# Performance work log

Hardware: AMD Instinct MI355X
Metric: run time of the kernel (lower is better)

## Reference

```python
import jax, jax.numpy as jnp
import numpy as np
import math

B, S, H = 2, 2048, 1024
NH, DK, DV = 16, 64, 64
PAD = 0
VOCAB = 32000


def setup_inputs() -> dict:
    key = jax.random.key(0)
    ks = jax.random.split(key, 6)
    batch = jax.random.normal(ks[0], (B, S, H), dtype=jnp.float32)
    input_ids = jax.random.randint(ks[1], (B, S), 1, VOCAB)
    n_pad = S // 20
    input_ids = input_ids.at[:, S - n_pad:].set(PAD)
    init = 1.0 / math.sqrt(H)  # xavier-ish scale
    W_Q = jax.random.normal(ks[2], (H, NH * DK), dtype=jnp.float32) * init
    W_K = jax.random.normal(ks[3], (H, NH * DK), dtype=jnp.float32) * init
    W_V = jax.random.normal(ks[4], (H, NH * DV), dtype=jnp.float32) * init
    W_O = jax.random.normal(ks[5], (NH * DV, H), dtype=jnp.float32) * init
    return {
        "batch": batch, "input_ids": input_ids,
        "W_Q": W_Q, "W_K": W_K, "W_V": W_V,
        "b_Q": jnp.zeros((NH * DK,), jnp.float32),
        "b_K": jnp.zeros((NH * DK,), jnp.float32),
        "b_V": jnp.zeros((NH * DV,), jnp.float32),
        "W_O": W_O, "b_O": jnp.zeros((H,), jnp.float32),
    }


def reference(batch, input_ids, W_Q, W_K, W_V, b_Q, b_K, b_V, W_O, b_O):
    Bn, Sn, _ = batch.shape
    NEG = jnp.float32(-jnp.inf)
    # causal mask [S,S]: 0 where i>=j else -inf
    i = jnp.arange(Sn)
    causal = jnp.where(i[:, None] >= i[None, :], 0.0, NEG).astype(batch.dtype)
    # padding mask [B,1,S]: -inf at pad key positions
    pad = jnp.where(input_ids == PAD, NEG, 0.0).astype(batch.dtype)
    mask = causal[None, :, :] + pad[:, None, :]  # [B,S,S]

    Q = (batch @ W_Q + b_Q).reshape(Bn, Sn, NH, DK)
    K = (batch @ W_K + b_K).reshape(Bn, Sn, NH, DK)
    V = (batch @ W_V + b_V).reshape(Bn, Sn, NH, DV)

    scores = jnp.einsum('bqhd,bkhd->bhqk', Q, K) / math.sqrt(DK)
    attn = jax.nn.softmax(scores + mask[:, None, :, :], axis=-1)
    out = jnp.einsum('bhqk,bkhd->bqhd', attn, V).reshape(Bn, Sn, NH * DV)
    return out @ W_O + b_O
```

## Files before the change

kernel.cpp:

```cpp
#include <hip/hip_runtime.h>
#include <stdint.h>


typedef unsigned short u16;
typedef __attribute__((ext_vector_type(8))) __bf16 bf16x8;
typedef __attribute__((ext_vector_type(4))) float f32x4;

#define SCL 0.18033688011112042f

__device__ __forceinline__ u16 f2bf(float f) {
  union { float f; uint32_t u; } v; v.f = f;
  uint32_t r = v.u + 0x7FFFu + ((v.u >> 16) & 1u);
  return (u16)(r >> 16);
}

__device__ __forceinline__ void gl_lds16(const u16* g, u16* l) {
  auto gp = reinterpret_cast<const __attribute__((address_space(1))) uint32_t*>(
      reinterpret_cast<uintptr_t>(g));
  auto lp = reinterpret_cast<__attribute__((address_space(3))) uint32_t*>(
      reinterpret_cast<uintptr_t>(l));
  __builtin_amdgcn_global_load_lds(gp, lp, 16, 0, 0);
}

__global__ void k_prologue(const float* __restrict__ batch, const int* __restrict__ ids,
                           const float* __restrict__ W_Q, const float* __restrict__ W_K,
                           const float* __restrict__ W_V, const float* __restrict__ W_O,
                           u16* __restrict__ Xbf, u16* __restrict__ dqkv, u16* __restrict__ dwo,
                           unsigned long long* __restrict__ pb) {
  __shared__ float tile[32][33];
  const int bx = blockIdx.x, t = threadIdx.x;
  if (bx < 4096) {
    int idx = (bx * 256 + t) * 4;
    const float4 v = *reinterpret_cast<const float4*>(batch + idx);
    uint2 o;
    o.x = (uint32_t)f2bf(v.x) | ((uint32_t)f2bf(v.y) << 16);
    o.y = (uint32_t)f2bf(v.z) | ((uint32_t)f2bf(v.w) << 16);
    *reinterpret_cast<uint2*>(Xbf + idx) = o;
  } else if (bx < 8192) {
    int b2 = bx - 4096;
    int z = b2 >> 10;
    b2 &= 1023;
    const float* src = z == 0 ? W_Q : (z == 1 ? W_K : (z == 2 ? W_V : W_O));
    u16* dst = z < 3 ? dqkv + (size_t)z * 1024 * 1024 : dwo;
    int c0 = (b2 & 31) * 32, r0 = (b2 >> 5) * 32;
    int tx = t & 31, ty = t >> 5;
#pragma unroll
    for (int i = 0; i < 4; ++i)
      tile[ty + i * 8][tx] = src[(size_t)(r0 + ty + i * 8) * 1024 + c0 + tx];
    __syncthreads();
#pragma unroll
    for (int i = 0; i < 4; ++i)
      dst[(size_t)(c0 + ty + i * 8) * 1024 + r0 + tx] = f2bf(tile[tx][ty + i * 8]);
  } else {
    int idx = (bx - 8192) * 4 + (t >> 6);
    int ln = t & 63;
    int b = idx >> 5, j = idx & 31;
    unsigned long long m = __ballot(ids[b * 2048 + j * 64 + ln] == 0);
    if (ln == 0) pb[idx] = m;
  }
}


__device__ __forceinline__ void gemm_tile_acc(
    const u16* __restrict__ A, const u16* __restrict__ Bt, int K,
    int tm, int tn, u16* As, u16* Bs, f32x4 acc[4][4]) {
  const int t = threadIdx.x, wv = t >> 6, ln = t & 63;
  const int wr = (wv & 1) * 64, wc = (wv >> 1) * 64;
  const int lr = ln & 15, q8 = (ln >> 4) * 8;
  const int srow = ln >> 2, scol = (ln & 3) * 8;

  for (int k0 = 0; k0 < K; k0 += 32) {
#pragma unroll
    for (int i = 0; i < 2; ++i) {
      int c = wv + i * 4;
      gl_lds16(A + (size_t)(tm + c * 16 + srow) * K + k0 + scol, As + c * 512 + ln * 8);
      gl_lds16(Bt + (size_t)(tn + c * 16 + srow) * K + k0 + scol, Bs + c * 512 + ln * 8);
    }
    __syncthreads();
    bf16x8 av[4], bv[4];
#pragma unroll
    for (int m = 0; m < 4; ++m)
      av[m] = *reinterpret_cast<const bf16x8*>(As + (wr + m * 16 + lr) * 32 + q8);
#pragma unroll
    for (int n = 0; n < 4; ++n)
      bv[n] = *reinterpret_cast<const bf16x8*>(Bs + (wc + n * 16 + lr) * 32 + q8);
#pragma unroll
    for (int m = 0; m < 4; ++m)
#pragma unroll
      for (int n = 0; n < 4; ++n)
        acc[m][n] = __builtin_amdgcn_mfma_f32_16x16x32_bf16(av[m], bv[n], acc[m][n], 0, 0, 0);
    __syncthreads();
  }
}

__global__ __launch_bounds__(256) void k_qkv(
    const u16* __restrict__ X, const u16* __restrict__ Wt,
    const float* __restrict__ bQ, const float* __restrict__ bK, const float* __restrict__ bV,
    u16* __restrict__ Qt, u16* __restrict__ Kt, u16* __restrict__ Vt) {
  __shared__ __align__(16) u16 As[128 * 32];
  __shared__ __align__(16) u16 Bs[128 * 32];
  f32x4 acc[4][4] = {};
  const int tm = blockIdx.x * 128, tn = blockIdx.y * 128;
  gemm_tile_acc(X, Wt, 1024, tm, tn, As, Bs, acc);

  const int t = threadIdx.x, wv = t >> 6, ln = t & 63;
  const int wr = (wv & 1) * 64, wc = (wv >> 1) * 64;
  const int lr = ln & 15, q4 = (ln >> 4) * 4;
  const int which = tn >> 10;

  if (which == 0) {
#pragma unroll
    for (int n = 0; n < 4; ++n) {
      int f = (tn + wc + n * 16 + lr) & 1023;
      float bb = bQ[f];
      int h = f >> 6, dd = f & 63;
      int kh = dd >> 5, qq = (dd & 31) >> 3, e = dd & 7;
#pragma unroll
      for (int m = 0; m < 4; ++m)
#pragma unroll
        for (int r = 0; r < 4; ++r) {
          int gr = tm + wr + m * 16 + q4 + r;
          int b = gr >> 11, s = gr & 2047;
          int bh = b * 16 + h;
          size_t addr = (((size_t)(bh * 64 + (s >> 5)) * 4 + ((s & 31) >> 4) * 2 + kh) << 9) +
                        ((s & 15) + 16 * qq) * 8 + e;
          Qt[addr] = f2bf((acc[m][n][r] + bb) * SCL);
        }
    }
  } else if (which == 1) {
#pragma unroll
    for (int n = 0; n < 4; ++n) {
      int f = (tn + wc + n * 16 + lr) & 1023;
      float bb = bK[f];
      int h = f >> 6, dd = f & 63;
      int kh = dd >> 5, qq = (dd & 31) >> 3, e = dd & 7;
#pragma unroll
      for (int m = 0; m < 4; ++m)
#pragma unroll
        for (int r = 0; r < 4; ++r) {
          int gr = tm + wr + m * 16 + q4 + r;
          int b = gr >> 11, s = gr & 2047;
          int bh = b * 16 + h;
          size_t addr = (((size_t)(bh * 32 + (s >> 6)) * 8 + kh * 4 + ((s & 63) >> 4)) << 9) +
                        ((s & 15) + 16 * qq) * 8 + e;
          Kt[addr] = f2bf(acc[m][n][r] + bb);
        }
    }
  } else {
#pragma unroll
    for (int n = 0; n < 4; ++n) {
      int f = (tn + wc + n * 16 + lr) & 1023;
      float bb = bV[f];
      int h = f >> 6, dd = f & 63;
      int md = dd >> 4, lrv = dd & 15;
#pragma unroll
      for (int m = 0; m < 4; ++m) {
        int gr0 = tm + wr + m * 16 + q4;
        int b = gr0 >> 11, s0 = gr0 & 2047;
        int bh = b * 16 + h;
        int j = s0 >> 6, kh = (s0 & 63) >> 5, qv = (s0 & 31) >> 3, e0 = s0 & 7;
        size_t addr = (((size_t)(bh * 32 + j) * 8 + kh * 4 + md) << 9) +
                      (lrv + 16 * qv) * 8 + e0;
        uint2 pk;
        pk.x = (uint32_t)f2bf(acc[m][n][0] + bb) | ((uint32_t)f2bf(acc[m][n][1] + bb) << 16);
        pk.y = (uint32_t)f2bf(acc[m][n][2] + bb) | ((uint32_t)f2bf(acc[m][n][3] + bb) << 16);
        *reinterpret_cast<uint2*>(Vt + addr) = pk;
      }
    }
  }
}

__global__ __launch_bounds__(256) void k_out(
    const u16* __restrict__ O, const u16* __restrict__ WoT,
    const float* __restrict__ bO, float* __restrict__ out) {
  __shared__ __align__(16) u16 As[128 * 32];
  __shared__ __align__(16) u16 Bs[128 * 32];
  f32x4 acc[4][4] = {};
  const int tm = blockIdx.x * 128, tn = blockIdx.y * 128;
  gemm_tile_acc(O, WoT, 1024, tm, tn, As, Bs, acc);

  const int t = threadIdx.x, wv = t >> 6, ln = t & 63;
  const int wr = (wv & 1) * 64, wc = (wv >> 1) * 64;
  const int lr = ln & 15, q4 = (ln >> 4) * 4;
#pragma unroll
  for (int n = 0; n < 4; ++n) {
    int gc = tn + wc + n * 16 + lr;
    float bb = bO[gc];
#pragma unroll
    for (int m = 0; m < 4; ++m)
#pragma unroll
      for (int r = 0; r < 4; ++r) {
        int gr = tm + wr + m * 16 + q4 + r;
        out[(size_t)gr * 1024 + gc] = acc[m][n][r] + bb;
      }
  }
}

__global__ __launch_bounds__(256, 3) void k_attn(
    const u16* __restrict__ Qt, const u16* __restrict__ Kt, const u16* __restrict__ Vt,
    const unsigned long long* __restrict__ padbits,
    u16* __restrict__ Opart, float* __restrict__ Lpart) {
  __shared__ __align__(16) u16 Ks[2][4096];
  __shared__ __align__(16) u16 Vs[2][4096];
  __shared__ __align__(16) u16 Ps[128 * 72];

  const int id = blockIdx.x;
  const int bh = id & 31;
  const int w = 39 - (id >> 5);
  int p, c;
  if (w < 4)       { p = w;                    c = 0; }
  else if (w < 12) { p = 4 + ((w - 4) >> 1);   c = (w - 4) & 1; }
  else if (w < 24) { p = 8 + (w - 12) / 3;     c = (w - 12) % 3; }
  else             { p = 12 + ((w - 24) >> 2); c = (w - 24) & 3; }
  const int jts = c * 8;
  const int jte = min(2 * p + 2, jts + 8);
  const int slot = bh * 40 + w;
  const int bI = bh >> 4;

  const int t = threadIdx.x, wv = t >> 6, ln = t & 63;
  const int lr = ln & 15, q4 = (ln >> 4) * 4, q8 = (ln >> 4) * 8;
  const int qbase = p * 128 + wv * 32;
  const int qrow = wv * 32;

  bf16x8 bq[2][2];
  {
    const u16* qb = Qt + (((size_t)(bh * 64 + (qbase >> 5)) * 4) << 9) + ln * 8;
#pragma unroll
    for (int n = 0; n < 2; ++n)
#pragma unroll
      for (int kh = 0; kh < 2; ++kh)
        bq[n][kh] = *reinterpret_cast<const bf16x8*>(qb + ((n * 2 + kh) << 9));
  }

  float lo[2] = {0.f, 0.f};
  f32x4 Oc[4][2] = {};

  const u16* Kg = Kt + (((size_t)bh * 32) << 12);
  const u16* Vg = Vt + (((size_t)bh * 32) << 12);
  const int st = t * 8;

#pragma unroll
  for (int r = 0; r < 2; ++r) {
    gl_lds16(Kg + (((size_t)jts) << 12) + st + r * 2048, &Ks[0][st + r * 2048]);
    gl_lds16(Vg + (((size_t)jts) << 12) + st + r * 2048, &Vs[0][st + r * 2048]);
  }
  __syncthreads();

  for (int j = jts; j < jte; ++j) {
    const int cur = (j - jts) & 1, nxt = cur ^ 1;
    if (j + 1 < jte) {
#pragma unroll
      for (int r = 0; r < 2; ++r) {
        gl_lds16(Kg + (((size_t)(j + 1)) << 12) + st + r * 2048, &Ks[nxt][st + r * 2048]);
        gl_lds16(Vg + (((size_t)(j + 1)) << 12) + st + r * 2048, &Vs[nxt][st + r * 2048]);
      }
    }

    const int kb = j * 64;
    const unsigned long long pb = padbits[bI * 32 + j];
    const bool masked = (kb + 63 > qbase) || (pb != 0);

    f32x4 sc[4][2] = {};
#pragma unroll
    for (int m = 0; m < 4; ++m) {
      const bf16x8 ak0 = *reinterpret_cast<const bf16x8*>(&Ks[cur][m * 512 + ln * 8]);
      const bf16x8 ak1 = *reinterpret_cast<const bf16x8*>(&Ks[cur][(4 + m) * 512 + ln * 8]);
#pragma unroll
      for (int n = 0; n < 2; ++n) {
        sc[m][n] = __builtin_amdgcn_mfma_f32_16x16x32_bf16(ak0, bq[n][0], sc[m][n], 0, 0, 0);
        sc[m][n] = __builtin_amdgcn_mfma_f32_16x16x32_bf16(ak1, bq[n][1], sc[m][n], 0, 0, 0);
      }
    }

#pragma unroll
    for (int n = 0; n < 2; ++n) {
      if (masked) {
        const int qabs = qbase + n * 16 + lr;
#pragma unroll
        for (int m = 0; m < 4; ++m)
#pragma unroll
          for (int r = 0; r < 4; ++r) {
            const int sl = m * 16 + q4 + r;
            const bool dead = (kb + sl > qabs) || ((pb >> sl) & 1ull);
            sc[m][n][r] = dead ? -1e30f : sc[m][n][r];
          }
      }
      float ps = 0.f;
#pragma unroll
      for (int m = 0; m < 4; ++m) {
        float p0 = exp2f(sc[m][n][0]);
        float p1 = exp2f(sc[m][n][1]);
        float p2 = exp2f(sc[m][n][2]);
        float p3 = exp2f(sc[m][n][3]);
        ps += (p0 + p1) + (p2 + p3);
        uint2 pk;
        pk.x = __builtin_amdgcn_perm(__float_as_uint(p1), __float_as_uint(p0), 0x07060302);
        pk.y = __builtin_amdgcn_perm(__float_as_uint(p3), __float_as_uint(p2), 0x07060302);
        *reinterpret_cast<uint2*>(Ps + (qrow + n * 16 + lr) * 72 + m * 16 + q4) = pk;
      }
      lo[n] += ps;
    }

    bf16x8 bp[2][2];
#pragma unroll
    for (int n = 0; n < 2; ++n) {
      bp[n][0] = *reinterpret_cast<const bf16x8*>(Ps + (qrow + n * 16 + lr) * 72 + q8);
      bp[n][1] = *reinterpret_cast<const bf16x8*>(Ps + (qrow + n * 16 + lr) * 72 + 32 + q8);
    }

#pragma unroll
    for (int md = 0; md < 4; ++md) {
      const bf16x8 av0 = *reinterpret_cast<const bf16x8*>(&Vs[cur][md * 512 + ln * 8]);
      const bf16x8 av1 = *reinterpret_cast<const bf16x8*>(&Vs[cur][(4 + md) * 512 + ln * 8]);
#pragma unroll
      for (int n = 0; n < 2; ++n) {
        Oc[md][n] = __builtin_amdgcn_mfma_f32_16x16x32_bf16(av0, bp[n][0], Oc[md][n], 0, 0, 0);
        Oc[md][n] = __builtin_amdgcn_mfma_f32_16x16x32_bf16(av1, bp[n][1], Oc[md][n], 0, 0, 0);
      }
    }

    if (j + 1 < jte) __syncthreads();
  }

  const size_t obase = (size_t)slot * 8192;
#pragma unroll
  for (int n = 0; n < 2; ++n) {
    lo[n] += __shfl_xor(lo[n], 16, 64);
    lo[n] += __shfl_xor(lo[n], 32, 64);
    const float inv = 1.f / lo[n];
    const int qlocal = qrow + n * 16 + lr;
#pragma unroll
    for (int md = 0; md < 4; ++md) {
      uint2 pk;
      pk.x = (uint32_t)f2bf(Oc[md][n][0] * inv) | ((uint32_t)f2bf(Oc[md][n][1] * inv) << 16);
      pk.y = (uint32_t)f2bf(Oc[md][n][2] * inv) | ((uint32_t)f2bf(Oc[md][n][3] * inv) << 16);
      *reinterpret_cast<uint2*>(Opart + obase + (size_t)qlocal * 64 + md * 16 + q4) = pk;
    }
    if (ln < 16) Lpart[slot * 128 + qlocal] = lo[n];
  }
}

__global__ __launch_bounds__(256) void k_merge(
    const u16* __restrict__ Opart, const float* __restrict__ Lpart, u16* __restrict__ O) {
  const int bh = blockIdx.x >> 5, sub = blockIdx.x & 31;
  const int p = sub >> 1, half = sub & 1;
  const int nc = p < 4 ? 1 : p < 8 ? 2 : p < 12 ? 3 : 4;
  const int pre = p < 4 ? p
               : p < 8 ? 4 + (p - 4) * 2
               : p < 12 ? 12 + (p - 8) * 3
               : 24 + (p - 12) * 4;
  const int slot0 = bh * 40 + pre;

  const int t = threadIdx.x;
  const int q = half * 64 + (t >> 2), ds = (t & 3) * 16;

  float wc[4], wsum = 0.f;
  for (int cI = 0; cI < nc; ++cI) {
    wc[cI] = Lpart[(slot0 + cI) * 128 + q];
    wsum += wc[cI];
  }
  const float inv = 1.f / wsum;

  float acc[16];
#pragma unroll
  for (int e = 0; e < 16; ++e) acc[e] = 0.f;
  for (int cI = 0; cI < nc; ++cI) {
    const u16* src = Opart + (size_t)(slot0 + cI) * 8192 + q * 64 + ds;
    uint4 a = *reinterpret_cast<const uint4*>(src);
    uint4 b = *reinterpret_cast<const uint4*>(src + 8);
    uint32_t uu[8] = {a.x, a.y, a.z, a.w, b.x, b.y, b.z, b.w};
    const float wci = wc[cI];
#pragma unroll
    for (int pp = 0; pp < 8; ++pp) {
      acc[2 * pp]     += wci * __uint_as_float(uu[pp] << 16);
      acc[2 * pp + 1] += wci * __uint_as_float(uu[pp] & 0xFFFF0000u);
    }
  }

  const int bI = bh >> 4, hI = bh & 15;
  const size_t row = (size_t)(bI * 2048 + p * 128 + q);
  u16* dst = O + row * 1024 + hI * 64 + ds;
  uint32_t op[8];
#pragma unroll
  for (int pp = 0; pp < 8; ++pp)
    op[pp] = (uint32_t)f2bf(acc[2 * pp] * inv) | ((uint32_t)f2bf(acc[2 * pp + 1] * inv) << 16);
  *reinterpret_cast<uint4*>(dst) = *reinterpret_cast<const uint4*>(&op[0]);
  *reinterpret_cast<uint4*>(dst + 8) = *reinterpret_cast<const uint4*>(&op[4]);
}


extern "C" void kernel_launch(void* const* d_in, const int* in_sizes, int n_in,
                              void* d_out, int out_size, void* d_ws, size_t ws_size,
                              hipStream_t stream) {
  (void)in_sizes; (void)n_in; (void)out_size; (void)ws_size;
  const float* batch = (const float*)d_in[0];
  const int* ids     = (const int*)d_in[1];
  const float* W_Q   = (const float*)d_in[2];
  const float* W_K   = (const float*)d_in[3];
  const float* W_V   = (const float*)d_in[4];
  const float* b_Q   = (const float*)d_in[5];
  const float* b_K   = (const float*)d_in[6];
  const float* b_V   = (const float*)d_in[7];
  const float* W_O   = (const float*)d_in[8];
  const float* b_O   = (const float*)d_in[9];
  float* out = (float*)d_out;

  u16* ws = (u16*)d_ws;
  u16* Xbf   = ws;
  u16* WqkvT = Xbf + 4194304;
  u16* WoT   = WqkvT + 3145728;
  u16* Qtb   = WoT + 1048576;
  u16* Ktb   = Qtb + 4194304;
  u16* Vtb   = Ktb + 4194304;
  u16* Opart = Vtb + 4194304;
  float* Lpart = (float*)WqkvT;
  u16* Ob    = Xbf;

  unsigned long long* padbits =
      (unsigned long long*)((char*)d_out + (size_t)out_size * 4 - 512);

  k_prologue<<<8208, 256, 0, stream>>>(batch, ids, W_Q, W_K, W_V, W_O, Xbf, WqkvT, WoT, padbits);
  k_qkv<<<dim3(32, 24), 256, 0, stream>>>(Xbf, WqkvT, b_Q, b_K, b_V, Qtb, Ktb, Vtb);
  k_attn<<<1280, 256, 0, stream>>>(Qtb, Ktb, Vtb, padbits, Opart, Lpart);
  k_merge<<<1024, 256, 0, stream>>>(Opart, Lpart, Ob);
  k_out<<<dim3(32, 8), 256, 0, stream>>>(Ob, WoT, b_O, out);
}
```

Measured before the change: 213.0 us.

## Keep softmax probabilities in registers and feed PV via 16x16x16 MFMA

Removes the LDS staging buffer for P by packing the bf16 probabilities directly into register operands and using 16x16x16 bf16 MFMAs, whose B-operand layout matches the score accumulator layout. The V transpose layout written by the projection kernel is changed so each 8-element load splits into two halves that match the new k ordering. Dropping the P shared buffer lowers LDS use, and the launch bound is raised to allow 5 blocks per CU. The cost is twice as many, smaller MFMA instructions and more register pressure under the tighter occupancy bound.

```diff
diff --git a/kernel.cpp b/kernel.cpp
--- a/kernel.cpp
+++ b/kernel.cpp
@@ -5,6 +5,7 @@
 typedef unsigned short u16;
 typedef __attribute__((ext_vector_type(8))) __bf16 bf16x8;
 typedef __attribute__((ext_vector_type(4))) float f32x4;
+typedef __attribute__((ext_vector_type(4))) short s16x4;
 
 #define SCL 0.18033688011112042f
 
@@ -152,15 +153,16 @@
       int f = (tn + wc + n * 16 + lr) & 1023;
       float bb = bV[f];
       int h = f >> 6, dd = f & 63;
-      int md = dd >> 4, lrv = dd & 15;
+      int md = dd >> 4, iv = dd & 15;
 #pragma unroll
       for (int m = 0; m < 4; ++m) {
         int gr0 = tm + wr + m * 16 + q4;
         int b = gr0 >> 11, s0 = gr0 & 2047;
         int bh = b * 16 + h;
-        int j = s0 >> 6, kh = (s0 & 63) >> 5, qv = (s0 & 31) >> 3, e0 = s0 & 7;
-        size_t addr = (((size_t)(bh * 32 + j) * 8 + kh * 4 + md) << 9) +
-                      (lrv + 16 * qv) * 8 + e0;
+        int j = s0 >> 6, k5 = s0 & 63;
+        int mp = k5 >> 5, g = (k5 & 15) >> 2, h0 = (k5 & 16) >> 2;
+        size_t addr = (((size_t)(bh * 32 + j) * 8 + mp * 4 + md) << 9) +
+                      (g * 16 + iv) * 8 + h0;
         uint2 pk;
         pk.x = (uint32_t)f2bf(acc[m][n][0] + bb) | ((uint32_t)f2bf(acc[m][n][1] + bb) << 16);
         pk.y = (uint32_t)f2bf(acc[m][n][2] + bb) | ((uint32_t)f2bf(acc[m][n][3] + bb) << 16);
@@ -196,13 +198,12 @@
   }
 }
 
-__global__ __launch_bounds__(256, 3) void k_attn(
+__global__ __launch_bounds__(256, 5) void k_attn(
     const u16* __restrict__ Qt, const u16* __restrict__ Kt, const u16* __restrict__ Vt,
     const unsigned long long* __restrict__ padbits,
     u16* __restrict__ Opart, float* __restrict__ Lpart) {
   __shared__ __align__(16) u16 Ks[2][4096];
   __shared__ __align__(16) u16 Vs[2][4096];
-  __shared__ __align__(16) u16 Ps[128 * 72];
 
   const int id = blockIdx.x;
   const int bh = id & 31;
@@ -218,7 +219,7 @@
   const int bI = bh >> 4;
 
   const int t = threadIdx.x, wv = t >> 6, ln = t & 63;
-  const int lr = ln & 15, q4 = (ln >> 4) * 4, q8 = (ln >> 4) * 8;
+  const int lr = ln & 15, q4 = (ln >> 4) * 4;
   const int qbase = p * 128 + wv * 32;
   const int qrow = wv * 32;
 
@@ -272,6 +273,7 @@
       }
     }
 
+    s16x4 pbf[4][2];
 #pragma unroll
     for (int n = 0; n < 2; ++n) {
       if (masked) {
@@ -293,31 +295,28 @@
         float p2 = exp2f(sc[m][n][2]);
         float p3 = exp2f(sc[m][n][3]);
         ps += (p0 + p1) + (p2 + p3);
-        uint2 pk;
-        pk.x = __builtin_amdgcn_perm(__float_as_uint(p1), __float_as_uint(p0), 0x07060302);
-        pk.y = __builtin_amdgcn_perm(__float_as_uint(p3), __float_as_uint(p2), 0x07060302);
-        *reinterpret_cast<uint2*>(Ps + (qrow + n * 16 + lr) * 72 + m * 16 + q4) = pk;
+        union { uint2 u; s16x4 s; } pu;
+        pu.u.x = __builtin_amdgcn_perm(__float_as_uint(p1), __float_as_uint(p0), 0x07060302);
+        pu.u.y = __builtin_amdgcn_perm(__float_as_uint(p3), __float_as_uint(p2), 0x07060302);
+        pbf[m][n] = pu.s;
       }
       lo[n] += ps;
     }
 
-    bf16x8 bp[2][2];
-#pragma unroll
-    for (int n = 0; n < 2; ++n) {
-      bp[n][0] = *reinterpret_cast<const bf16x8*>(Ps + (qrow + n * 16 + lr) * 72 + q8);
-      bp[n][1] = *reinterpret_cast<const bf16x8*>(Ps + (qrow + n * 16 + lr) * 72 + 32 + q8);
-    }
-
-#pragma unroll
-    for (int md = 0; md < 4; ++md) {
-      const bf16x8 av0 = *reinterpret_cast<const bf16x8*>(&Vs[cur][md * 512 + ln * 8]);
-      const bf16x8 av1 = *reinterpret_cast<const bf16x8*>(&Vs[cur][(4 + md) * 512 + ln * 8]);
-#pragma unroll
-      for (int n = 0; n < 2; ++n) {
-        Oc[md][n] = __builtin_amdgcn_mfma_f32_16x16x32_bf16(av0, bp[n][0], Oc[md][n], 0, 0, 0);
-        Oc[md][n] = __builtin_amdgcn_mfma_f32_16x16x32_bf16(av1, bp[n][1], Oc[md][n], 0, 0, 0);
-      }
-    }
+#pragma unroll
+    for (int mp = 0; mp < 2; ++mp)
+#pragma unroll
+      for (int md = 0; md < 4; ++md) {
+        union { bf16x8 v; struct { s16x4 lo, hi; } s; } vu;
+        vu.v = *reinterpret_cast<const bf16x8*>(&Vs[cur][(mp * 4 + md) * 512 + ln * 8]);
+#pragma unroll
+        for (int n = 0; n < 2; ++n) {
+          Oc[md][n] = __builtin_amdgcn_mfma_f32_16x16x16bf16_1k(
+              vu.s.lo, pbf[2 * mp][n], Oc[md][n], 0, 0, 0);
+          Oc[md][n] = __builtin_amdgcn_mfma_f32_16x16x16bf16_1k(
+              vu.s.hi, pbf[2 * mp + 1][n], Oc[md][n], 0, 0, 0);
+        }
+      }
 
     if (j + 1 < jte) __syncthreads();
   }
```

Measured after the change: 355.2 us. 1.67x slower.
